# Optimization experiments

Hardware: AMD Instinct MI355X
Metric: run time of the kernel (lower is better)

The kernel has to match this reference:

```python
import jax, jax.numpy as jnp
import numpy as np

N_NODES = 10000
N_EDGES = 160000
F_IN, D, N_CLS = 300, 1024, 10
NEG_SLOPE = 0.2


def setup_inputs() -> dict:
    key = jax.random.key(0)
    ks = jax.random.split(key, 12)
    s = 0.05  # small init scale for numerical sanity
    return {
        "x": jax.random.normal(ks[0], (N_NODES, F_IN), jnp.float32),
        "edge_index": jax.random.randint(ks[1], (2, N_EDGES), 0, N_NODES, jnp.int64),
        "W1": jax.random.normal(ks[2], (F_IN, D), jnp.float32) * s,
        "att_src1": jax.random.normal(ks[3], (D,), jnp.float32) * s,
        "att_dst1": jax.random.normal(ks[4], (D,), jnp.float32) * s,
        "b1": jnp.zeros((D,), jnp.float32),
        "W2": jax.random.normal(ks[5], (D, D), jnp.float32) * s,
        "att_src2": jax.random.normal(ks[6], (D,), jnp.float32) * s,
        "att_dst2": jax.random.normal(ks[7], (D,), jnp.float32) * s,
        "b2": jnp.zeros((D,), jnp.float32),
        "fc_w": jax.random.normal(ks[8], (D, N_CLS), jnp.float32) * s,
        "fc_b": jnp.zeros((N_CLS,), jnp.float32),
    }


def gat_conv(x, src, dst, W, a_src, a_dst, b):
    # PyG GATConv, heads=1: h = x W; e_ij = leaky_relu(a_src.h_j + a_dst.h_i)
    h = x @ W                      # [N, D]
    e = jax.nn.leaky_relu((h @ a_src)[src] + (h @ a_dst)[dst], NEG_SLOPE)  # [E]
    # scatter-softmax over edges grouped by destination node
    m = jax.lax.stop_gradient(jax.ops.segment_max(e, dst, num_segments=N_NODES))
    ex = jnp.exp(e - m[dst])
    denom = jax.ops.segment_sum(ex, dst, num_segments=N_NODES)
    alpha = ex / denom[dst]        # [E]
    out = jax.ops.segment_sum(alpha[:, None] * h[src], dst, num_segments=N_NODES)
    return out + b


def reference(x, edge_index, W1, att_src1, att_dst1, b1,
              W2, att_src2, att_dst2, b2, fc_w, fc_b):
    loops = jnp.arange(N_NODES, dtype=edge_index.dtype)
    src = jnp.concatenate([edge_index[0], loops])  # add_self_loops=True
    dst = jnp.concatenate([edge_index[1], loops])
    emb = jax.nn.relu(gat_conv(x, src, dst, W1, att_src1, att_dst1, b1))
    emb = jax.nn.relu(gat_conv(emb, src, dst, W2, att_src2, att_dst2, b2))
    return jax.nn.softmax(emb @ fc_w + fc_b, axis=-1)
```

## Files before the change

kernel.cpp:

```cpp
#include <hip/hip_runtime.h>
#include <hip/hip_bf16.h>
#include <hip/hip_fp16.h>
#include <math.h>

#define N_NODES 10000
#define N_EDGES 160000
#define E_TOT   (N_EDGES + N_NODES)
#define F_IN    300
#define D       1024
#define N_CLS   10
#define NEG_SLOPE 0.2f

#define MP      10112
#define KP1     320
#define KP2     1024

typedef __attribute__((ext_vector_type(8))) _Float16 f16x8;
typedef __attribute__((ext_vector_type(4))) _Float16 f16x4;
typedef __attribute__((ext_vector_type(4))) float f32x4;

#define GLOAD_LDS16(g, l) __builtin_amdgcn_global_load_lds( \
    (const __attribute__((address_space(1))) void*)(g), \
    (__attribute__((address_space(3))) void*)(l), 16, 0, 0)


__global__ void init_deg(int* __restrict__ deg) {
    int i = blockIdx.x * blockDim.x + threadIdx.x;
    if (i < N_NODES) deg[i] = 1;
}

__global__ void count_edges(const int* __restrict__ dst, int* __restrict__ deg) {
    int e = blockIdx.x * blockDim.x + threadIdx.x;
    if (e < N_EDGES) atomicAdd(&deg[dst[e]], 1);
}

__global__ void scan_offs(const int* __restrict__ deg, int* __restrict__ offs,
                          int* __restrict__ pos) {
    __shared__ int sbuf[1024];
    __shared__ int scarry;
    int t = threadIdx.x;
    if (t == 0) { scarry = 0; offs[0] = 0; }
    __syncthreads();
    for (int base = 0; base < N_NODES; base += 1024) {
        int v = (base + t < N_NODES) ? deg[base + t] : 0;
        sbuf[t] = v;
        __syncthreads();
        for (int off = 1; off < 1024; off <<= 1) {
            int add = (t >= off) ? sbuf[t - off] : 0;
            __syncthreads();
            sbuf[t] += add;
            __syncthreads();
        }
        int carry = scarry;
        if (base + t < N_NODES) {
            int incl = carry + sbuf[t];
            offs[base + t + 1] = incl;
            pos[base + t]      = incl - v;
        }
        __syncthreads();
        if (t == 1023) scarry = carry + sbuf[1023];
        __syncthreads();
    }
}

__global__ void scatter_edges(const int* __restrict__ src, const int* __restrict__ dst,
                              int* __restrict__ pos, int* __restrict__ ssrc) {
    int e = blockIdx.x * blockDim.x + threadIdx.x;
    if (e < N_EDGES) {
        int d = dst[e];
        int p = atomicAdd(&pos[d], 1);
        ssrc[p] = src[e];
    } else if (e < E_TOT) {
        int i = e - N_EDGES;
        int p = atomicAdd(&pos[i], 1);
        ssrc[p] = i;
    }
}


__global__ void prep_uv(const float* __restrict__ W1, const float* __restrict__ as1,
                        const float* __restrict__ ad1, const float* __restrict__ W2,
                        const float* __restrict__ as2, const float* __restrict__ ad2,
                        float* __restrict__ u1, float* __restrict__ v1,
                        float* __restrict__ u2, float* __restrict__ v2) {
    int wid  = (int)((blockIdx.x * blockDim.x + threadIdx.x) >> 6);
    int lane = threadIdx.x & 63;
    const float* row;
    const float* a;
    const float* b;
    float *du, *dv;
    int k;
    if (wid < F_IN) {
        k = wid; row = W1 + (size_t)k * D; a = as1; b = ad1; du = u1; dv = v1;
    } else if (wid < F_IN + D) {
        k = wid - F_IN; row = W2 + (size_t)k * D; a = as2; b = ad2; du = u2; dv = v2;
    } else return;
    float s1 = 0.f, s2 = 0.f;
    for (int n = lane; n < D; n += 64) {
        float w = row[n];
        s1 += w * a[n];
        s2 += w * b[n];
    }
    #pragma unroll
    for (int o = 32; o; o >>= 1) { s1 += __shfl_xor(s1, o); s2 += __shfl_xor(s2, o); }
    if (lane == 0) { du[k] = s1; dv[k] = s2; }
}


__global__ void node_scores_x(const float* __restrict__ x, const float* __restrict__ u1,
                              const float* __restrict__ v1, float* __restrict__ hs,
                              float* __restrict__ hd) {
    int wid  = (int)((blockIdx.x * blockDim.x + threadIdx.x) >> 6);
    int lane = threadIdx.x & 63;
    if (wid >= N_NODES) return;
    const float* row = x + (size_t)wid * F_IN;
    float s1 = 0.f, s2 = 0.f;
    for (int k = lane; k < F_IN; k += 64) {
        float v = row[k];
        s1 += v * u1[k];
        s2 += v * v1[k];
    }
    #pragma unroll
    for (int o = 32; o; o >>= 1) { s1 += __shfl_xor(s1, o); s2 += __shfl_xor(s2, o); }
    if (lane == 0) { hs[wid] = s1; hd[wid] = s2; }
}


#define ZR1 (112 * KP1)
#define ZR2 (N_NODES * 20)
#define ZR3 (112 * KP2)
#define ZTOT (2*ZR1 + 2*ZR2 + 2*ZR3 + 2*N_NODES)

__global__ void zero_misc(float* __restrict__ hs2, float* __restrict__ hd2,
                          unsigned short* __restrict__ Ah1, unsigned short* __restrict__ Al1,
                          unsigned short* __restrict__ Ah2, unsigned short* __restrict__ Al2) {
    int idx = blockIdx.x * blockDim.x + threadIdx.x;
    if (idx >= ZTOT) return;
    if (idx < 2 * ZR1) {
        unsigned short* B = (idx < ZR1) ? Ah1 : Al1;
        int off = (idx < ZR1) ? idx : idx - ZR1;
        B[(size_t)N_NODES * KP1 + off] = 0;
    } else if ((idx -= 2 * ZR1) < 2 * ZR2) {
        unsigned short* B = (idx < ZR2) ? Ah1 : Al1;
        int off = (idx < ZR2) ? idx : idx - ZR2;
        int r = off / 20, c = 300 + off % 20;
        B[(size_t)r * KP1 + c] = 0;
    } else if ((idx -= 2 * ZR2) < 2 * ZR3) {
        unsigned short* B = (idx < ZR3) ? Ah2 : Al2;
        int off = (idx < ZR3) ? idx : idx - ZR3;
        B[(size_t)N_NODES * KP2 + off] = 0;
    } else {
        idx -= 2 * ZR3;
        if (idx < N_NODES) hs2[idx] = 0.f;
        else hd2[idx - N_NODES] = 0.f;
    }
}


__global__ void transpose_f16(const float* __restrict__ W, _Float16* __restrict__ BTh,
                              int K, int N, int Kp) {
    __shared__ float tile[32][33];
    int k0 = blockIdx.x * 32, n0 = blockIdx.y * 32;
    int tx = threadIdx.x, ty = threadIdx.y;
    #pragma unroll
    for (int j = 0; j < 32; j += 8) {
        int k = k0 + ty + j;
        tile[ty + j][tx] = (k < K) ? W[(size_t)k * N + n0 + tx] : 0.f;
    }
    __syncthreads();
    #pragma unroll
    for (int j = 0; j < 32; j += 8) {
        int n = n0 + ty + j;
        int k = k0 + tx;
        BTh[(size_t)n * Kp + k] = (_Float16)tile[tx][ty + j];
    }
}


__global__ __launch_bounds__(256) void aggregate_x(
        const float* __restrict__ x, const float* __restrict__ hs,
        const float* __restrict__ hd, const int* __restrict__ offs,
        const int* __restrict__ ssrc, _Float16* __restrict__ outh,
        _Float16* __restrict__ outl) {
    int i = blockIdx.x;
    int t = threadIdx.x;
    int lane = t & 63;
    int wv = t >> 6;
    int start = offs[i], end = offs[i + 1];
    __shared__ float red[8];
    __shared__ float part[2][75][4];
    float hdi = hd[i];

    float lmax = -INFINITY;
    for (int p = start + t; p < end; p += 256) {
        float s = hs[ssrc[p]] + hdi;
        s = (s >= 0.f) ? s : s * NEG_SLOPE;
        lmax = fmaxf(lmax, s);
    }
    #pragma unroll
    for (int o = 32; o; o >>= 1) lmax = fmaxf(lmax, __shfl_xor(lmax, o));
    if (lane == 0) red[wv] = lmax;
    __syncthreads();
    float m = fmaxf(fmaxf(red[0], red[1]), fmaxf(red[2], red[3]));

    float lsum = 0.f;
    for (int p = start + t; p < end; p += 256) {
        float s = hs[ssrc[p]] + hdi;
        s = (s >= 0.f) ? s : s * NEG_SLOPE;
        lsum += __expf(s - m);
    }
    #pragma unroll
    for (int o = 32; o; o >>= 1) lsum += __shfl_xor(lsum, o);
    if (lane == 0) red[4 + wv] = lsum;
    __syncthreads();
    float inv = 1.0f / (red[4] + red[5] + red[6] + red[7]);

    int g = t / 75;
    int s = t - g * 75;
    int c = s * 4;
    float4 a = {0.f, 0.f, 0.f, 0.f};
    if (t < 225) {
        int p = start + g;
        for (; p + 3 < end; p += 6) {
            int j0 = ssrc[p], j1 = ssrc[p + 3];
            float s0 = hs[j0] + hdi; s0 = (s0 >= 0.f) ? s0 : s0 * NEG_SLOPE;
            float s1 = hs[j1] + hdi; s1 = (s1 >= 0.f) ? s1 : s1 * NEG_SLOPE;
            float w0 = __expf(s0 - m), w1 = __expf(s1 - m);
            float4 v0 = *(const float4*)(x + (size_t)j0 * F_IN + c);
            float4 v1 = *(const float4*)(x + (size_t)j1 * F_IN + c);
            a.x += w0 * v0.x + w1 * v1.x;
            a.y += w0 * v0.y + w1 * v1.y;
            a.z += w0 * v0.z + w1 * v1.z;
            a.w += w0 * v0.w + w1 * v1.w;
        }
        if (p < end) {
            int j0 = ssrc[p];
            float s0 = hs[j0] + hdi; s0 = (s0 >= 0.f) ? s0 : s0 * NEG_SLOPE;
            float w0 = __expf(s0 - m);
            float4 v0 = *(const float4*)(x + (size_t)j0 * F_IN + c);
            a.x += w0 * v0.x; a.y += w0 * v0.y; a.z += w0 * v0.z; a.w += w0 * v0.w;
        }
    }
    if (t < 225 && g > 0) {
        part[g - 1][s][0] = a.x; part[g - 1][s][1] = a.y;
        part[g - 1][s][2] = a.z; part[g - 1][s][3] = a.w;
    }
    __syncthreads();
    if (t < 75) {
        a.x += part[0][t][0] + part[1][t][0];
        a.y += part[0][t][1] + part[1][t][1];
        a.z += part[0][t][2] + part[1][t][2];
        a.w += part[0][t][3] + part[1][t][3];
        float rv[4] = {a.x * inv, a.y * inv, a.z * inv, a.w * inv};
        _Float16 hi4[4], lo4[4];
        #pragma unroll
        for (int q = 0; q < 4; ++q) {
            _Float16 hi = (_Float16)rv[q];
            hi4[q] = hi;
            lo4[q] = (_Float16)(rv[q] - (float)hi);
        }
        *(float2*)(outh + (size_t)i * KP1 + c) = *(float2*)hi4;
        *(float2*)(outl + (size_t)i * KP1 + c) = *(float2*)lo4;
    }
}


__global__ __launch_bounds__(256) void aggregate_d(
        const _Float16* __restrict__ h, const float* __restrict__ hs,
        const float* __restrict__ hd, const int* __restrict__ offs,
        const int* __restrict__ ssrc, _Float16* __restrict__ outh,
        _Float16* __restrict__ outl) {
    int i = blockIdx.x;
    int t = threadIdx.x;
    int lane = t & 63;
    int wv = t >> 6;
    int start = offs[i], end = offs[i + 1];
    __shared__ float red[8];
    float hdi = hd[i];

    float lmax = -INFINITY;
    for (int p = start + t; p < end; p += 256) {
        float s = hs[ssrc[p]] + hdi;
        s = (s >= 0.f) ? s : s * NEG_SLOPE;
        lmax = fmaxf(lmax, s);
    }
    #pragma unroll
    for (int o = 32; o; o >>= 1) lmax = fmaxf(lmax, __shfl_xor(lmax, o));
    if (lane == 0) red[wv] = lmax;
    __syncthreads();
    float m = fmaxf(fmaxf(red[0], red[1]), fmaxf(red[2], red[3]));

    float lsum = 0.f;
    for (int p = start + t; p < end; p += 256) {
        float s = hs[ssrc[p]] + hdi;
        s = (s >= 0.f) ? s : s * NEG_SLOPE;
        lsum += __expf(s - m);
    }
    #pragma unroll
    for (int o = 32; o; o >>= 1) lsum += __shfl_xor(lsum, o);
    if (lane == 0) red[4 + wv] = lsum;
    __syncthreads();
    float inv = 1.0f / (red[4] + red[5] + red[6] + red[7]);

    int c = t * 4;
    float4 a0 = {0.f,0.f,0.f,0.f}, a1 = a0, a2 = a0, a3 = a0;
    int p = start;
    for (; p + 4 <= end; p += 4) {
        int j0 = ssrc[p], j1 = ssrc[p+1], j2 = ssrc[p+2], j3 = ssrc[p+3];
        float s0 = hs[j0] + hdi; s0 = (s0 >= 0.f) ? s0 : s0 * NEG_SLOPE;
        float s1 = hs[j1] + hdi; s1 = (s1 >= 0.f) ? s1 : s1 * NEG_SLOPE;
        float s2 = hs[j2] + hdi; s2 = (s2 >= 0.f) ? s2 : s2 * NEG_SLOPE;
        float s3 = hs[j3] + hdi; s3 = (s3 >= 0.f) ? s3 : s3 * NEG_SLOPE;
        float w0 = __expf(s0 - m), w1 = __expf(s1 - m);
        float w2 = __expf(s2 - m), w3 = __expf(s3 - m);
        f16x4 v0 = *(const f16x4*)(h + (size_t)j0 * D + c);
        f16x4 v1 = *(const f16x4*)(h + (size_t)j1 * D + c);
        f16x4 v2 = *(const f16x4*)(h + (size_t)j2 * D + c);
        f16x4 v3 = *(const f16x4*)(h + (size_t)j3 * D + c);
        a0.x += w0*(float)v0.x; a0.y += w0*(float)v0.y; a0.z += w0*(float)v0.z; a0.w += w0*(float)v0.w;
        a1.x += w1*(float)v1.x; a1.y += w1*(float)v1.y; a1.z += w1*(float)v1.z; a1.w += w1*(float)v1.w;
        a2.x += w2*(float)v2.x; a2.y += w2*(float)v2.y; a2.z += w2*(float)v2.z; a2.w += w2*(float)v2.w;
        a3.x += w3*(float)v3.x; a3.y += w3*(float)v3.y; a3.z += w3*(float)v3.z; a3.w += w3*(float)v3.w;
    }
    for (; p < end; ++p) {
        int j0 = ssrc[p];
        float s0 = hs[j0] + hdi; s0 = (s0 >= 0.f) ? s0 : s0 * NEG_SLOPE;
        float w0 = __expf(s0 - m);
        f16x4 v0 = *(const f16x4*)(h + (size_t)j0 * D + c);
        a0.x += w0*(float)v0.x; a0.y += w0*(float)v0.y; a0.z += w0*(float)v0.z; a0.w += w0*(float)v0.w;
    }
    float rv[4];
    rv[0] = ((a0.x + a1.x) + (a2.x + a3.x)) * inv;
    rv[1] = ((a0.y + a1.y) + (a2.y + a3.y)) * inv;
    rv[2] = ((a0.z + a1.z) + (a2.z + a3.z)) * inv;
    rv[3] = ((a0.w + a1.w) + (a2.w + a3.w)) * inv;
    _Float16 hi4[4], lo4[4];
    #pragma unroll
    for (int q = 0; q < 4; ++q) {
        _Float16 hi = (_Float16)rv[q];
        hi4[q] = hi;
        lo4[q] = (_Float16)(rv[q] - (float)hi);
    }
    *(float2*)(outh + (size_t)i * KP2 + c) = *(float2*)hi4;
    *(float2*)(outl + (size_t)i * KP2 + c) = *(float2*)lo4;
}


__global__ __launch_bounds__(256) void gemm_split_mfma(
        const _Float16* __restrict__ Ah, const _Float16* __restrict__ Al,
        const _Float16* __restrict__ BTh,
        float* __restrict__ Cf, _Float16* __restrict__ Ch,
        const float* __restrict__ bias,
        const float* __restrict__ asrc, const float* __restrict__ adst,
        float* __restrict__ hs, float* __restrict__ hd,
        int Mreal, int Kp, int dots) {
    __shared__ char lds[49152];
    const int t    = threadIdx.x;
    const int lane = t & 63;
    const int wid  = t >> 6;
    const int chunkg = (int)gridDim.x >> 3;
    const int vid  = ((int)blockIdx.x & 7) * chunkg + ((int)blockIdx.x >> 3);
    const int n0 = (vid & 7) * 128;
    const int m0 = (vid >> 3) * 128;
    const int wr = (wid >> 1) * 64;
    const int wc = (wid & 1) * 64;
    const int fr = lane & 15;
    const int kg = lane >> 4;

    const int r0 = t >> 2, s0 = t & 3;
    const int r1 = r0 + 64;
    const int g0 = (s0 ^ ((r0 >> 1) & 3)) << 3;
    const int g1 = (s0 ^ ((r1 >> 1) & 3)) << 3;
    const size_t oA0 = (size_t)(m0 + r0) * Kp + g0;
    const size_t oA1 = (size_t)(m0 + r1) * Kp + g1;
    const size_t oB0 = (size_t)(n0 + r0) * Kp + g0;
    const size_t oB1 = (size_t)(n0 + r1) * Kp + g1;
    const int ko = (kg ^ ((fr >> 1) & 3)) << 4;

    f32x4 acc[4][4] = {};

    auto STAGE = [&](int b, int kb) {
        char* base = lds + b * 24576;
        GLOAD_LDS16(Ah  + oA0 + kb, base + t * 16);
        GLOAD_LDS16(Ah  + oA1 + kb, base + 4096  + t * 16);
        GLOAD_LDS16(Al  + oA0 + kb, base + 8192  + t * 16);
        GLOAD_LDS16(Al  + oA1 + kb, base + 12288 + t * 16);
        GLOAD_LDS16(BTh + oB0 + kb, base + 16384 + t * 16);
        GLOAD_LDS16(BTh + oB1 + kb, base + 20480 + t * 16);
    };

    STAGE(0, 0);
    __syncthreads();

    int cur = 0;
    for (int kb = 0; kb < Kp; kb += 32) {
        if (kb + 32 < Kp) STAGE(cur ^ 1, kb + 32);
        char* base = lds + cur * 24576;
        f16x8 ah[4], al[4], bh[4];
        #pragma unroll
        for (int f = 0; f < 4; ++f) {
            int ra = (wr + f * 16 + fr) * 64 + ko;
            int rb = (wc + f * 16 + fr) * 64 + ko;
            ah[f] = *(const f16x8*)(base + ra);
            al[f] = *(const f16x8*)(base + 8192 + ra);
            bh[f] = *(const f16x8*)(base + 16384 + rb);
        }
        #pragma unroll
        for (int fm = 0; fm < 4; ++fm)
            #pragma unroll
            for (int fn = 0; fn < 4; ++fn)
                acc[fm][fn] = __builtin_amdgcn_mfma_f32_16x16x32_f16(
                    ah[fm], bh[fn], acc[fm][fn], 0, 0, 0);
        #pragma unroll
        for (int fm = 0; fm < 4; ++fm)
            #pragma unroll
            for (int fn = 0; fn < 4; ++fn)
                acc[fm][fn] = __builtin_amdgcn_mfma_f32_16x16x32_f16(
                    al[fm], bh[fn], acc[fm][fn], 0, 0, 0);
        __syncthreads();
        cur ^= 1;
    }

    float bv[4];
    #pragma unroll
    for (int fn = 0; fn < 4; ++fn) bv[fn] = bias[n0 + wc + fn * 16 + fr];
    #pragma unroll
    for (int fm = 0; fm < 4; ++fm) {
        int mb = m0 + wr + fm * 16 + kg * 4;
        #pragma unroll
        for (int fn = 0; fn < 4; ++fn) {
            int cn = n0 + wc + fn * 16 + fr;
            #pragma unroll
            for (int j = 0; j < 4; ++j) {
                float r = fmaxf(acc[fm][fn][j] + bv[fn], 0.f);
                acc[fm][fn][j] = r;
                int m = mb + j;
                if (m < Mreal) {
                    if (Cf) Cf[(size_t)m * 1024 + cn] = r;
                    else    Ch[(size_t)m * 1024 + cn] = (_Float16)r;
                }
            }
        }
    }

    if (dots) {
        float av[4], dv[4];
        #pragma unroll
        for (int fn = 0; fn < 4; ++fn) {
            int cn = n0 + wc + fn * 16 + fr;
            av[fn] = asrc[cn];
            dv[fn] = adst[cn];
        }
        #pragma unroll
        for (int fm = 0; fm < 4; ++fm) {
            #pragma unroll
            for (int j = 0; j < 4; ++j) {
                float v1 = acc[fm][0][j] * av[0] + acc[fm][1][j] * av[1]
                         + acc[fm][2][j] * av[2] + acc[fm][3][j] * av[3];
                float v2 = acc[fm][0][j] * dv[0] + acc[fm][1][j] * dv[1]
                         + acc[fm][2][j] * dv[2] + acc[fm][3][j] * dv[3];
                #pragma unroll
                for (int o = 1; o < 16; o <<= 1) {
                    v1 += __shfl_xor(v1, o);
                    v2 += __shfl_xor(v2, o);
                }
                int m = m0 + wr + fm * 16 + kg * 4 + j;
                if (fr == 0 && m < Mreal) {
                    atomicAdd(&hs[m], v1);
                    atomicAdd(&hd[m], v2);
                }
            }
        }
    }
}


__global__ void fc_softmax(const float* __restrict__ emb, const float* __restrict__ fcw,
                           const float* __restrict__ fcb, float* __restrict__ out) {
    int wid  = (int)((blockIdx.x * blockDim.x + threadIdx.x) >> 6);
    int lane = threadIdx.x & 63;
    if (wid >= N_NODES) return;
    float acc[N_CLS] = {};
    const float* row = emb + (size_t)wid * D;
    for (int k = lane * 4; k < D; k += 256) {
        float4 v = *(const float4*)(row + k);
        #pragma unroll
        for (int c = 0; c < N_CLS; ++c)
            acc[c] += v.x * fcw[k * N_CLS + c] + v.y * fcw[(k+1) * N_CLS + c]
                    + v.z * fcw[(k+2) * N_CLS + c] + v.w * fcw[(k+3) * N_CLS + c];
    }
    #pragma unroll
    for (int c = 0; c < N_CLS; ++c) {
        #pragma unroll
        for (int o = 32; o; o >>= 1) acc[c] += __shfl_xor(acc[c], o);
    }
    if (lane == 0) {
        float logit[N_CLS];
        float m = -INFINITY;
        #pragma unroll
        for (int c = 0; c < N_CLS; ++c) { logit[c] = acc[c] + fcb[c]; m = fmaxf(m, logit[c]); }
        float s = 0.f;
        #pragma unroll
        for (int c = 0; c < N_CLS; ++c) { logit[c] = __expf(logit[c] - m); s += logit[c]; }
        float invs = 1.0f / s;
        #pragma unroll
        for (int c = 0; c < N_CLS; ++c) out[(size_t)wid * N_CLS + c] = logit[c] * invs;
    }
}


extern "C" void kernel_launch(void* const* d_in, const int* in_sizes, int n_in,
                              void* d_out, int out_size, void* d_ws, size_t ws_size,
                              hipStream_t stream) {
    const float* x        = (const float*)d_in[0];
    const int*   ei       = (const int*)d_in[1];
    const float* W1       = (const float*)d_in[2];
    const float* att_src1 = (const float*)d_in[3];
    const float* att_dst1 = (const float*)d_in[4];
    const float* b1       = (const float*)d_in[5];
    const float* W2       = (const float*)d_in[6];
    const float* att_src2 = (const float*)d_in[7];
    const float* att_dst2 = (const float*)d_in[8];
    const float* b2       = (const float*)d_in[9];
    const float* fc_w     = (const float*)d_in[10];
    const float* fc_b     = (const float*)d_in[11];
    float* out = (float*)d_out;

    const int* src = ei;
    const int* dst = ei + N_EDGES;

    char* w = (char*)d_ws;
    #define ALLOC(name, bytes) char* name = w; w += (((size_t)(bytes) + 255) & ~(size_t)255)
    ALLOC(p_emb,   (size_t)N_NODES * D * 4);
    ALLOC(p_embh,  (size_t)N_NODES * D * 2);
    ALLOC(p_hs1,   (size_t)N_NODES * 4);
    ALLOC(p_hd1,   (size_t)N_NODES * 4);
    ALLOC(p_hs2,   (size_t)N_NODES * 4);
    ALLOC(p_hd2,   (size_t)N_NODES * 4);
    ALLOC(p_deg,   (size_t)N_NODES * 4);
    ALLOC(p_offs,  (size_t)(N_NODES + 1) * 4);
    ALLOC(p_pos,   (size_t)N_NODES * 4);
    ALLOC(p_ssrc,  (size_t)E_TOT * 4);
    ALLOC(p_u1,    (size_t)F_IN * 4);
    ALLOC(p_v1,    (size_t)F_IN * 4);
    ALLOC(p_u2,    (size_t)D * 4);
    ALLOC(p_v2,    (size_t)D * 4);
    ALLOC(p_as1,   (size_t)2 * MP * KP1 * 2);
    ALLOC(p_as2,   (size_t)2 * MP * KP2 * 2);
    ALLOC(p_bt1,   (size_t)D * KP1 * 2);
    ALLOC(p_bt2,   (size_t)D * KP2 * 2);
    #undef ALLOC

    float* emb  = (float*)p_emb;
    _Float16* embh = (_Float16*)p_embh;
    float* hs1  = (float*)p_hs1;
    float* hd1  = (float*)p_hd1;
    float* hs2  = (float*)p_hs2;
    float* hd2  = (float*)p_hd2;
    int*   deg  = (int*)p_deg;
    int*   offs = (int*)p_offs;
    int*   pos  = (int*)p_pos;
    int*   ssrc = (int*)p_ssrc;
    float* u1 = (float*)p_u1; float* v1 = (float*)p_v1;
    float* u2 = (float*)p_u2; float* v2 = (float*)p_v2;
    _Float16* Ah1  = (_Float16*)p_as1;
    _Float16* Al1  = Ah1 + (size_t)MP * KP1;
    _Float16* Ah2  = (_Float16*)p_as2;
    _Float16* Al2  = Ah2 + (size_t)MP * KP2;
    _Float16* BT1h = (_Float16*)p_bt1;
    _Float16* BT2h = (_Float16*)p_bt2;

    init_deg<<<(N_NODES + 255) / 256, 256, 0, stream>>>(deg);
    count_edges<<<(N_EDGES + 255) / 256, 256, 0, stream>>>(dst, deg);
    scan_offs<<<1, 1024, 0, stream>>>(deg, offs, pos);
    scatter_edges<<<(E_TOT + 255) / 256, 256, 0, stream>>>(src, dst, pos, ssrc);

    prep_uv<<<((F_IN + D) * 64 + 255) / 256, 256, 0, stream>>>(
        W1, att_src1, att_dst1, W2, att_src2, att_dst2, u1, v1, u2, v2);
    dim3 tb(32, 8);
    transpose_f16<<<dim3(KP1 / 32, D / 32), tb, 0, stream>>>(W1, BT1h, F_IN, D, KP1);
    transpose_f16<<<dim3(KP2 / 32, D / 32), tb, 0, stream>>>(W2, BT2h, D, D, KP2);
    zero_misc<<<(ZTOT + 255) / 256, 256, 0, stream>>>(hs2, hd2,
        (unsigned short*)Ah1, (unsigned short*)Al1,
        (unsigned short*)Ah2, (unsigned short*)Al2);

    const int gemmGrid = (D / 128) * (MP / 128);

    node_scores_x<<<(N_NODES * 64 + 255) / 256, 256, 0, stream>>>(x, u1, v1, hs1, hd1);
    aggregate_x<<<N_NODES, 256, 0, stream>>>(x, hs1, hd1, offs, ssrc, Ah1, Al1);
    gemm_split_mfma<<<gemmGrid, 256, 0, stream>>>(Ah1, Al1, BT1h,
                                                  (float*)nullptr, embh, b1,
                                                  u2, v2, hs2, hd2, N_NODES, KP1, 1);

    aggregate_d<<<N_NODES, 256, 0, stream>>>(embh, hs2, hd2, offs, ssrc, Ah2, Al2);
    gemm_split_mfma<<<gemmGrid, 256, 0, stream>>>(Ah2, Al2, BT2h,
                                                  emb, (_Float16*)nullptr, b2,
                                                  (const float*)nullptr, (const float*)nullptr,
                                                  (float*)nullptr, (float*)nullptr,
                                                  N_NODES, KP2, 0);

    fc_softmax<<<(N_NODES * 64 + 255) / 256, 256, 0, stream>>>(emb, fc_w, fc_b, out);
}
```

Before: 338.4 us.

## Fuse prep kernels, widen aggregate_d loads, store layer-2 output in fp16

```diff
diff --git a/kernel.cpp b/kernel.cpp
--- a/kernel.cpp
+++ b/kernel.cpp
@@ -16,18 +16,12 @@
 #define KP2     1024
 
 typedef __attribute__((ext_vector_type(8))) _Float16 f16x8;
-typedef __attribute__((ext_vector_type(4))) _Float16 f16x4;
 typedef __attribute__((ext_vector_type(4))) float f32x4;
 
 #define GLOAD_LDS16(g, l) __builtin_amdgcn_global_load_lds( \
     (const __attribute__((address_space(1))) void*)(g), \
     (__attribute__((address_space(3))) void*)(l), 16, 0, 0)
 
-
-__global__ void init_deg(int* __restrict__ deg) {
-    int i = blockIdx.x * blockDim.x + threadIdx.x;
-    if (i < N_NODES) deg[i] = 1;
-}
 
 __global__ void count_edges(const int* __restrict__ dst, int* __restrict__ deg) {
     int e = blockIdx.x * blockDim.x + threadIdx.x;
@@ -78,64 +72,85 @@
 }
 
 
-__global__ void prep_uv(const float* __restrict__ W1, const float* __restrict__ as1,
-                        const float* __restrict__ ad1, const float* __restrict__ W2,
-                        const float* __restrict__ as2, const float* __restrict__ ad2,
-                        float* __restrict__ u1, float* __restrict__ v1,
-                        float* __restrict__ u2, float* __restrict__ v2) {
-    int wid  = (int)((blockIdx.x * blockDim.x + threadIdx.x) >> 6);
-    int lane = threadIdx.x & 63;
-    const float* row;
-    const float* a;
-    const float* b;
-    float *du, *dv;
-    int k;
-    if (wid < F_IN) {
-        k = wid; row = W1 + (size_t)k * D; a = as1; b = ad1; du = u1; dv = v1;
-    } else if (wid < F_IN + D) {
-        k = wid - F_IN; row = W2 + (size_t)k * D; a = as2; b = ad2; du = u2; dv = v2;
-    } else return;
-    float s1 = 0.f, s2 = 0.f;
-    for (int n = lane; n < D; n += 64) {
-        float w = row[n];
-        s1 += w * a[n];
-        s2 += w * b[n];
-    }
-    #pragma unroll
-    for (int o = 32; o; o >>= 1) { s1 += __shfl_xor(s1, o); s2 += __shfl_xor(s2, o); }
-    if (lane == 0) { du[k] = s1; dv[k] = s2; }
-}
-
-
-__global__ void node_scores_x(const float* __restrict__ x, const float* __restrict__ u1,
-                              const float* __restrict__ v1, float* __restrict__ hs,
-                              float* __restrict__ hd) {
-    int wid  = (int)((blockIdx.x * blockDim.x + threadIdx.x) >> 6);
-    int lane = threadIdx.x & 63;
-    if (wid >= N_NODES) return;
-    const float* row = x + (size_t)wid * F_IN;
-    float s1 = 0.f, s2 = 0.f;
-    for (int k = lane; k < F_IN; k += 64) {
-        float v = row[k];
-        s1 += v * u1[k];
-        s2 += v * v1[k];
-    }
-    #pragma unroll
-    for (int o = 32; o; o >>= 1) { s1 += __shfl_xor(s1, o); s2 += __shfl_xor(s2, o); }
-    if (lane == 0) { hs[wid] = s1; hd[wid] = s2; }
-}
-
-
 #define ZR1 (112 * KP1)
 #define ZR2 (N_NODES * 20)
 #define ZR3 (112 * KP2)
 #define ZTOT (2*ZR1 + 2*ZR2 + 2*ZR3 + 2*N_NODES)
 
-__global__ void zero_misc(float* __restrict__ hs2, float* __restrict__ hd2,
-                          unsigned short* __restrict__ Ah1, unsigned short* __restrict__ Al1,
-                          unsigned short* __restrict__ Ah2, unsigned short* __restrict__ Al2) {
-    int idx = blockIdx.x * blockDim.x + threadIdx.x;
-    if (idx >= ZTOT) return;
+#define ZONE_A 331
+#define ZONE_B 320
+#define ZONE_C 1024
+#define ZONE_D ((ZTOT + N_NODES + 255) / 256)
+
+__global__ __launch_bounds__(256) void mega_prep(
+        const float* __restrict__ W1, const float* __restrict__ as1,
+        const float* __restrict__ ad1, const float* __restrict__ W2,
+        const float* __restrict__ as2, const float* __restrict__ ad2,
+        float* __restrict__ u1, float* __restrict__ v1,
+        float* __restrict__ u2, float* __restrict__ v2,
+        _Float16* __restrict__ BT1h, _Float16* __restrict__ BT2h,
+        float* __restrict__ hs2, float* __restrict__ hd2,
+        unsigned short* __restrict__ Ah1, unsigned short* __restrict__ Al1,
+        unsigned short* __restrict__ Ah2, unsigned short* __restrict__ Al2,
+        int* __restrict__ deg) {
+    __shared__ float tile[32][33];
+    int b = blockIdx.x;
+    int t = threadIdx.x;
+
+    if (b < ZONE_A) {
+        int wid  = (b * 256 + t) >> 6;
+        int lane = t & 63;
+        const float* row; const float* a; const float* bb; float *du, *dv; int k;
+        if (wid < F_IN) {
+            k = wid; row = W1 + (size_t)k * D; a = as1; bb = ad1; du = u1; dv = v1;
+        } else {
+            k = wid - F_IN; row = W2 + (size_t)k * D; a = as2; bb = ad2; du = u2; dv = v2;
+        }
+        float s1 = 0.f, s2 = 0.f;
+        for (int n = lane; n < D; n += 64) {
+            float w = row[n];
+            s1 += w * a[n];
+            s2 += w * bb[n];
+        }
+        #pragma unroll
+        for (int o = 32; o; o >>= 1) { s1 += __shfl_xor(s1, o); s2 += __shfl_xor(s2, o); }
+        if (lane == 0) { du[k] = s1; dv[k] = s2; }
+        return;
+    }
+    if (b < ZONE_A + ZONE_B + ZONE_C) {
+        const float* W; _Float16* BT; int K, Kp, b2;
+        if (b < ZONE_A + ZONE_B) { b2 = b - ZONE_A; W = W1; BT = BT1h; K = F_IN; Kp = KP1;
+            int kb = b2 % (KP1 / 32), nb = b2 / (KP1 / 32);
+            int k0 = kb * 32, n0 = nb * 32;
+            int tx = t & 31, ty = t >> 5;
+            #pragma unroll
+            for (int j = 0; j < 32; j += 8) {
+                int k = k0 + ty + j;
+                tile[ty + j][tx] = (k < K) ? W[(size_t)k * D + n0 + tx] : 0.f;
+            }
+            __syncthreads();
+            #pragma unroll
+            for (int j = 0; j < 32; j += 8)
+                BT[(size_t)(n0 + ty + j) * Kp + k0 + tx] = (_Float16)tile[tx][ty + j];
+        } else { b2 = b - ZONE_A - ZONE_B; W = W2; BT = BT2h; K = D; Kp = KP2;
+            int kb = b2 & 31, nb = b2 >> 5;
+            int k0 = kb * 32, n0 = nb * 32;
+            int tx = t & 31, ty = t >> 5;
+            #pragma unroll
+            for (int j = 0; j < 32; j += 8) {
+                int k = k0 + ty + j;
+                tile[ty + j][tx] = (k < K) ? W[(size_t)k * D + n0 + tx] : 0.f;
+            }
+            __syncthreads();
+            #pragma unroll
+            for (int j = 0; j < 32; j += 8)
+                BT[(size_t)(n0 + ty + j) * Kp + k0 + tx] = (_Float16)tile[tx][ty + j];
+        }
+        return;
+    }
+    int idx = (b - ZONE_A - ZONE_B - ZONE_C) * 256 + t;
+    if (idx >= ZTOT + N_NODES) return;
+    if (idx >= ZTOT) { deg[idx - ZTOT] = 1; return; }
     if (idx < 2 * ZR1) {
         unsigned short* B = (idx < ZR1) ? Ah1 : Al1;
         int off = (idx < ZR1) ? idx : idx - ZR1;
@@ -157,23 +172,22 @@
 }
 
 
-__global__ void transpose_f16(const float* __restrict__ W, _Float16* __restrict__ BTh,
-                              int K, int N, int Kp) {
-    __shared__ float tile[32][33];
-    int k0 = blockIdx.x * 32, n0 = blockIdx.y * 32;
-    int tx = threadIdx.x, ty = threadIdx.y;
-    #pragma unroll
-    for (int j = 0; j < 32; j += 8) {
-        int k = k0 + ty + j;
-        tile[ty + j][tx] = (k < K) ? W[(size_t)k * N + n0 + tx] : 0.f;
-    }
-    __syncthreads();
-    #pragma unroll
-    for (int j = 0; j < 32; j += 8) {
-        int n = n0 + ty + j;
-        int k = k0 + tx;
-        BTh[(size_t)n * Kp + k] = (_Float16)tile[tx][ty + j];
-    }
+__global__ void node_scores_x(const float* __restrict__ x, const float* __restrict__ u1,
+                              const float* __restrict__ v1, float* __restrict__ hs,
+                              float* __restrict__ hd) {
+    int wid  = (int)((blockIdx.x * blockDim.x + threadIdx.x) >> 6);
+    int lane = threadIdx.x & 63;
+    if (wid >= N_NODES) return;
+    const float* row = x + (size_t)wid * F_IN;
+    float s1 = 0.f, s2 = 0.f;
+    for (int k = lane; k < F_IN; k += 64) {
+        float v = row[k];
+        s1 += v * u1[k];
+        s2 += v * v1[k];
+    }
+    #pragma unroll
+    for (int o = 32; o; o >>= 1) { s1 += __shfl_xor(s1, o); s2 += __shfl_xor(s2, o); }
+    if (lane == 0) { hs[wid] = s1; hd[wid] = s2; }
 }
 
 
@@ -276,6 +290,7 @@
     int wv = t >> 6;
     int start = offs[i], end = offs[i + 1];
     __shared__ float red[8];
+    __shared__ float part[128][8];
     float hdi = hd[i];
 
     float lmax = -INFINITY;
@@ -302,47 +317,59 @@
     __syncthreads();
     float inv = 1.0f / (red[4] + red[5] + red[6] + red[7]);
 
-    int c = t * 4;
-    float4 a0 = {0.f,0.f,0.f,0.f}, a1 = a0, a2 = a0, a3 = a0;
-    int p = start;
-    for (; p + 4 <= end; p += 4) {
-        int j0 = ssrc[p], j1 = ssrc[p+1], j2 = ssrc[p+2], j3 = ssrc[p+3];
+    int g = t >> 7;
+    int s = t & 127;
+    int c = s * 8;
+    float a0[8] = {}, a1[8] = {}, a2[8] = {}, a3[8] = {};
+    int p = start + g;
+    for (; p + 6 < end; p += 8) {
+        int j0 = ssrc[p], j1 = ssrc[p + 2], j2 = ssrc[p + 4], j3 = ssrc[p + 6];
         float s0 = hs[j0] + hdi; s0 = (s0 >= 0.f) ? s0 : s0 * NEG_SLOPE;
         float s1 = hs[j1] + hdi; s1 = (s1 >= 0.f) ? s1 : s1 * NEG_SLOPE;
         float s2 = hs[j2] + hdi; s2 = (s2 >= 0.f) ? s2 : s2 * NEG_SLOPE;
         float s3 = hs[j3] + hdi; s3 = (s3 >= 0.f) ? s3 : s3 * NEG_SLOPE;
         float w0 = __expf(s0 - m), w1 = __expf(s1 - m);
         float w2 = __expf(s2 - m), w3 = __expf(s3 - m);
-        f16x4 v0 = *(const f16x4*)(h + (size_t)j0 * D + c);
-        f16x4 v1 = *(const f16x4*)(h + (size_t)j1 * D + c);
-        f16x4 v2 = *(const f16x4*)(h + (size_t)j2 * D + c);
-        f16x4 v3 = *(const f16x4*)(h + (size_t)j3 * D + c);
-        a0.x += w0*(float)v0.x; a0.y += w0*(float)v0.y; a0.z += w0*(float)v0.z; a0.w += w0*(float)v0.w;
-        a1.x += w1*(float)v1.x; a1.y += w1*(float)v1.y; a1.z += w1*(float)v1.z; a1.w += w1*(float)v1.w;
-        a2.x += w2*(float)v2.x; a2.y += w2*(float)v2.y; a2.z += w2*(float)v2.z; a2.w += w2*(float)v2.w;
-        a3.x += w3*(float)v3.x; a3.y += w3*(float)v3.y; a3.z += w3*(float)v3.z; a3.w += w3*(float)v3.w;
-    }
-    for (; p < end; ++p) {
+        f16x8 v0 = *(const f16x8*)(h + (size_t)j0 * D + c);
+        f16x8 v1 = *(const f16x8*)(h + (size_t)j1 * D + c);
+        f16x8 v2 = *(const f16x8*)(h + (size_t)j2 * D + c);
+        f16x8 v3 = *(const f16x8*)(h + (size_t)j3 * D + c);
+        #pragma unroll
+        for (int q = 0; q < 8; ++q) {
+            a0[q] += w0 * (float)v0[q];
+            a1[q] += w1 * (float)v1[q];
+            a2[q] += w2 * (float)v2[q];
+            a3[q] += w3 * (float)v3[q];
+        }
+    }
+    for (; p < end; p += 2) {
         int j0 = ssrc[p];
         float s0 = hs[j0] + hdi; s0 = (s0 >= 0.f) ? s0 : s0 * NEG_SLOPE;
         float w0 = __expf(s0 - m);
-        f16x4 v0 = *(const f16x4*)(h + (size_t)j0 * D + c);
-        a0.x += w0*(float)v0.x; a0.y += w0*(float)v0.y; a0.z += w0*(float)v0.z; a0.w += w0*(float)v0.w;
-    }
-    float rv[4];
-    rv[0] = ((a0.x + a1.x) + (a2.x + a3.x)) * inv;
-    rv[1] = ((a0.y + a1.y) + (a2.y + a3.y)) * inv;
-    rv[2] = ((a0.z + a1.z) + (a2.z + a3.z)) * inv;
-    rv[3] = ((a0.w + a1.w) + (a2.w + a3.w)) * inv;
-    _Float16 hi4[4], lo4[4];
-    #pragma unroll
-    for (int q = 0; q < 4; ++q) {
-        _Float16 hi = (_Float16)rv[q];
-        hi4[q] = hi;
-        lo4[q] = (_Float16)(rv[q] - (float)hi);
-    }
-    *(float2*)(outh + (size_t)i * KP2 + c) = *(float2*)hi4;
-    *(float2*)(outl + (size_t)i * KP2 + c) = *(float2*)lo4;
+        f16x8 v0 = *(const f16x8*)(h + (size_t)j0 * D + c);
+        #pragma unroll
+        for (int q = 0; q < 8; ++q) a0[q] += w0 * (float)v0[q];
+    }
+    float af[8];
+    #pragma unroll
+    for (int q = 0; q < 8; ++q) af[q] = (a0[q] + a1[q]) + (a2[q] + a3[q]);
+    if (g == 1) {
+        #pragma unroll
+        for (int q = 0; q < 8; ++q) part[s][q] = af[q];
+    }
+    __syncthreads();
+    if (t < 128) {
+        _Float16 hi8[8], lo8[8];
+        #pragma unroll
+        for (int q = 0; q < 8; ++q) {
+            float rv = (af[q] + part[t][q]) * inv;
+            _Float16 hi = (_Float16)rv;
+            hi8[q] = hi;
+            lo8[q] = (_Float16)(rv - (float)hi);
+        }
+        *(float4*)(outh + (size_t)i * KP2 + c) = *(float4*)hi8;
+        *(float4*)(outl + (size_t)i * KP2 + c) = *(float4*)lo8;
+    }
 }
 
 
@@ -475,19 +502,21 @@
 }
 
 
-__global__ void fc_softmax(const float* __restrict__ emb, const float* __restrict__ fcw,
+__global__ void fc_softmax(const _Float16* __restrict__ emb, const float* __restrict__ fcw,
                            const float* __restrict__ fcb, float* __restrict__ out) {
     int wid  = (int)((blockIdx.x * blockDim.x + threadIdx.x) >> 6);
     int lane = threadIdx.x & 63;
     if (wid >= N_NODES) return;
     float acc[N_CLS] = {};
-    const float* row = emb + (size_t)wid * D;
-    for (int k = lane * 4; k < D; k += 256) {
-        float4 v = *(const float4*)(row + k);
-        #pragma unroll
-        for (int c = 0; c < N_CLS; ++c)
-            acc[c] += v.x * fcw[k * N_CLS + c] + v.y * fcw[(k+1) * N_CLS + c]
-                    + v.z * fcw[(k+2) * N_CLS + c] + v.w * fcw[(k+3) * N_CLS + c];
+    const _Float16* row = emb + (size_t)wid * D;
+    for (int k = lane * 8; k < D; k += 512) {
+        f16x8 v = *(const f16x8*)(row + k);
+        #pragma unroll
+        for (int q = 0; q < 8; ++q) {
+            float vv = (float)v[q];
+            #pragma unroll
+            for (int c = 0; c < N_CLS; ++c) acc[c] += vv * fcw[(k + q) * N_CLS + c];
+        }
     }
     #pragma unroll
     for (int c = 0; c < N_CLS; ++c) {
@@ -531,8 +560,8 @@
 
     char* w = (char*)d_ws;
     #define ALLOC(name, bytes) char* name = w; w += (((size_t)(bytes) + 255) & ~(size_t)255)
-    ALLOC(p_emb,   (size_t)N_NODES * D * 4);
-    ALLOC(p_embh,  (size_t)N_NODES * D * 2);
+    ALLOC(p_emb1h, (size_t)N_NODES * D * 2);
+    ALLOC(p_emb2h, (size_t)N_NODES * D * 2);
     ALLOC(p_hs1,   (size_t)N_NODES * 4);
     ALLOC(p_hd1,   (size_t)N_NODES * 4);
     ALLOC(p_hs2,   (size_t)N_NODES * 4);
@@ -551,8 +580,8 @@
     ALLOC(p_bt2,   (size_t)D * KP2 * 2);
     #undef ALLOC
 
-    float* emb  = (float*)p_emb;
-    _Float16* embh = (_Float16*)p_embh;
+    _Float16* emb1h = (_Float16*)p_emb1h;
+    _Float16* emb2h = (_Float16*)p_emb2h;
     float* hs1  = (float*)p_hs1;
     float* hd1  = (float*)p_hd1;
     float* hs2  = (float*)p_hs2;
@@ -570,34 +599,30 @@
     _Float16* BT1h = (_Float16*)p_bt1;
     _Float16* BT2h = (_Float16*)p_bt2;
 
-    init_deg<<<(N_NODES + 255) / 256, 256, 0, stream>>>(deg);
+    mega_prep<<<ZONE_A + ZONE_B + ZONE_C + ZONE_D, 256, 0, stream>>>(
+        W1, att_src1, att_dst1, W2, att_src2, att_dst2,
+        u1, v1, u2, v2, BT1h, BT2h, hs2, hd2,
+        (unsigned short*)Ah1, (unsigned short*)Al1,
+        (unsigned short*)Ah2, (unsigned short*)Al2, deg);
+
     count_edges<<<(N_EDGES + 255) / 256, 256, 0, stream>>>(dst, deg);
     scan_offs<<<1, 1024, 0, stream>>>(deg, offs, pos);
     scatter_edges<<<(E_TOT + 255) / 256, 256, 0, stream>>>(src, dst, pos, ssrc);
 
-    prep_uv<<<((F_IN + D) * 64 + 255) / 256, 256, 0, stream>>>(
-        W1, att_src1, att_dst1, W2, att_src2, att_dst2, u1, v1, u2, v2);
-    dim3 tb(32, 8);
-    transpose_f16<<<dim3(KP1 / 32, D / 32), tb, 0, stream>>>(W1, BT1h, F_IN, D, KP1);
-    transpose_f16<<<dim3(KP2 / 32, D / 32), tb, 0, stream>>>(W2, BT2h, D, D, KP2);
-    zero_misc<<<(ZTOT + 255) / 256, 256, 0, stream>>>(hs2, hd2,
-        (unsigned short*)Ah1, (unsigned short*)Al1,
-        (unsigned short*)Ah2, (unsigned short*)Al2);
-
     const int gemmGrid = (D / 128) * (MP / 128);
 
     node_scores_x<<<(N_NODES * 64 + 255) / 256, 256, 0, stream>>>(x, u1, v1, hs1, hd1);
     aggregate_x<<<N_NODES, 256, 0, stream>>>(x, hs1, hd1, offs, ssrc, Ah1, Al1);
     gemm_split_mfma<<<gemmGrid, 256, 0, stream>>>(Ah1, Al1, BT1h,
-                                                  (float*)nullptr, embh, b1,
+                                                  (float*)nullptr, emb1h, b1,
                                                   u2, v2, hs2, hd2, N_NODES, KP1, 1);
 
-    aggregate_d<<<N_NODES, 256, 0, stream>>>(embh, hs2, hd2, offs, ssrc, Ah2, Al2);
+    aggregate_d<<<N_NODES, 256, 0, stream>>>(emb1h, hs2, hd2, offs, ssrc, Ah2, Al2);
     gemm_split_mfma<<<gemmGrid, 256, 0, stream>>>(Ah2, Al2, BT2h,
-                                                  emb, (_Float16*)nullptr, b2,
+                                                  (float*)nullptr, emb2h, b2,
                                                   (const float*)nullptr, (const float*)nullptr,
                                                   (float*)nullptr, (float*)nullptr,
                                                   N_NODES, KP2, 0);
 
-    fc_softmax<<<(N_NODES * 64 + 255) / 256, 256, 0, stream>>>(emb, fc_w, fc_b, out);
-}
+    fc_softmax<<<(N_NODES * 64 + 255) / 256, 256, 0, stream>>>(emb2h, fc_w, fc_b, out);
+}
```

Measured after the change: 332.3 us. No clear change (-1.8%).
